# Optimization experiments

Measured on AMD Instinct MI355X. Metric: run time of the kernel, lower is better.

The kernel has to match this reference:

```python
import jax, jax.numpy as jnp
import numpy as np

NJ, NS = 30000, 12000            # num job / skill nodes
E_JS, E_SJ, E_SS = 300000, 300000, 150000
SBERT, HID, OUT = 384, 128, 128
H = 2                             # GAT heads (concat=True)
NEG_SLOPE = 0.2


def setup_inputs() -> dict:
    key = jax.random.key(0)
    ks = iter(jax.random.split(key, 64))
    nrm = lambda shape, s=1.0: jax.random.normal(next(ks), shape, jnp.float32) * s
    ridx = lambda n, hi: jax.random.randint(next(ks), (n,), 0, hi, jnp.int32)
    W = 0.05  # weight scale to keep activations sane across layers
    return dict(
        x_job=nrm((NJ, SBERT)), x_skill=nrm((NS, SBERT)),
        ei_js_src=ridx(E_JS, NJ), ei_js_dst=ridx(E_JS, NS),
        ei_sj_src=ridx(E_SJ, NS), ei_sj_dst=ridx(E_SJ, NJ),
        ei_ss_src=ridx(E_SS, NS), ei_ss_dst=ridx(E_SS, NS),
        query=nrm((SBERT,)),
        W0_job=nrm((SBERT, HID), W), b0_job=jnp.zeros((HID,), jnp.float32),
        g0_job=jnp.ones((HID,), jnp.float32), be0_job=jnp.zeros((HID,), jnp.float32),
        W0_skill=nrm((SBERT, HID), W), b0_skill=jnp.zeros((HID,), jnp.float32),
        g0_skill=jnp.ones((HID,), jnp.float32), be0_skill=jnp.zeros((HID,), jnp.float32),
        gat_Ws=nrm((2, 3, HID, H * HID), W), gat_Wd=nrm((2, 3, HID, H * HID), W),
        gat_as=nrm((2, 3, H, HID), W), gat_ad=nrm((2, 3, H, HID), W),
        gat_b=jnp.zeros((2, 3, H * HID), jnp.float32),
        inter_W=nrm((2, 2, H * HID, HID), W), inter_b=jnp.zeros((2, 2, HID), jnp.float32),
        Wjf=nrm((HID, OUT), W), bjf=jnp.zeros((OUT,), jnp.float32),
        Wq=nrm((SBERT, OUT), W), bq=jnp.zeros((OUT,), jnp.float32),
    )


def _layer_norm(x, g, b):
    mu = x.mean(-1, keepdims=True)
    var = ((x - mu) ** 2).mean(-1, keepdims=True)
    return (x - mu) * jax.lax.rsqrt(var + 1e-5) * g + b


def _gat(x_src, x_dst, src, dst, Ws, Wd, a_s, a_d, bias, num_dst):
    # PyG GATConv: lin_src/lin_dst (no bias), additive attention, scatter-softmax over dst.
    hs = (x_src @ Ws).reshape(-1, H, HID)            # [Ns,H,C]
    hd = (x_dst @ Wd).reshape(-1, H, HID)            # [Nd,H,C]
    e = jax.nn.leaky_relu((hs * a_s).sum(-1)[src] + (hd * a_d).sum(-1)[dst], NEG_SLOPE)  # [E,H]
    m = jax.ops.segment_max(e, dst, num_segments=num_dst)
    p = jnp.exp(e - m[dst])
    den = jax.ops.segment_sum(p, dst, num_segments=num_dst)
    w = p / (den[dst] + 1e-16)                       # [E,H]
    out = jax.ops.segment_sum(hs[src] * w[:, :, None], dst, num_segments=num_dst)
    return out.reshape(num_dst, H * HID) + bias


def _forward(x_job, x_skill, query,
             W0_job, b0_job, g0_job, be0_job, W0_skill, b0_skill, g0_skill, be0_skill,
             gat_Ws, gat_Wd, gat_as, gat_ad, gat_b, inter_W, inter_b, Wjf, bjf, Wq, bq,
             ei_js_src, ei_js_dst, ei_sj_src, ei_sj_dst, ei_ss_src, ei_ss_dst):
    # initial per-type lin + LN + relu (dropout = identity in eval)
    xj = jax.nn.relu(_layer_norm(x_job @ W0_job + b0_job, g0_job, be0_job))
    xs = jax.nn.relu(_layer_norm(x_skill @ W0_skill + b0_skill, g0_skill, be0_skill))
    # skill->skill relation adds self loops (src == dst node type)
    loops = jnp.arange(NS, dtype=jnp.int32)
    ss_src = jnp.concatenate([ei_ss_src, loops])
    ss_dst = jnp.concatenate([ei_ss_dst, loops])
    for i in range(2):  # num_layers
        o_s = (_gat(xj, xs, ei_js_src, ei_js_dst, gat_Ws[i, 0], gat_Wd[i, 0],
                    gat_as[i, 0], gat_ad[i, 0], gat_b[i, 0], NS)
               + _gat(xs, xs, ss_src, ss_dst, gat_Ws[i, 2], gat_Wd[i, 2],
                      gat_as[i, 2], gat_ad[i, 2], gat_b[i, 2], NS))  # HeteroConv aggr='sum'
        o_j = _gat(xs, xj, ei_sj_src, ei_sj_dst, gat_Ws[i, 1], gat_Wd[i, 1],
                   gat_as[i, 1], gat_ad[i, 1], gat_b[i, 1], NJ)
        xj = jax.nn.relu(o_j @ inter_W[i, 0] + inter_b[i, 0])
        xs = jax.nn.relu(o_s @ inter_W[i, 1] + inter_b[i, 1])
    job_emb = xj @ Wjf + bjf                          # [NJ,OUT]
    q = query @ Wq + bq                               # [OUT]
    scores = job_emb @ q                              # [NJ]
    return scores, job_emb, q


def reference(x_job, x_skill, ei_js_src, ei_js_dst, ei_sj_src, ei_sj_dst,
              ei_ss_src, ei_ss_dst, query,
              W0_job, b0_job, g0_job, be0_job, W0_skill, b0_skill, g0_skill, be0_skill,
              gat_Ws, gat_Wd, gat_as, gat_ad, gat_b, inter_W, inter_b,
              Wjf, bjf, Wq, bq):
    return _forward(x_job, x_skill, query,
                    W0_job, b0_job, g0_job, be0_job, W0_skill, b0_skill, g0_skill, be0_skill,
                    gat_Ws, gat_Wd, gat_as, gat_ad, gat_b, inter_W, inter_b, Wjf, bjf, Wq, bq,
                    ei_js_src, ei_js_dst, ei_sj_src, ei_sj_dst, ei_ss_src, ei_ss_dst)
```

## Files before the change

### kernel.cpp

```cpp
#include <hip/hip_runtime.h>
#include <hip/hip_bf16.h>
#include <math.h>

#define NJ 30000
#define NS 12000
#define E_JS 300000
#define E_SJ 300000
#define E_SS 150000
#define ETOT (E_JS + E_SJ + E_SS + NS)
#define NBINS (NS + NJ + NS)
#define NBUK ((NBINS + 63) / 64)
#define SBERT 384
#define HIST_NB 512
#define SCAT_NB 480
#define CAST_MATS 14
#define CAST_BPM 48
#define PREP_CAST (CAST_MATS * CAST_BPM)
#define PREP_WA   (PREP_CAST + 192)
#define PREP_QV   PREP_WA
#define PREP_GB   (PREP_QV + 1)
#define PREP_HIST (PREP_GB + 1)

static inline int cdiv(int a, int b) { return (a + b - 1) / b; }

typedef __attribute__((ext_vector_type(8))) short bf8_t;
typedef __attribute__((ext_vector_type(4))) float f4_t;
typedef unsigned short u16;

__device__ inline float bf2f(unsigned short u) {
    union { unsigned int i; float f; } z; z.i = ((unsigned int)u) << 16; return z.f;
}
__device__ inline unsigned short f2bf(float f) {
    unsigned int x = __float_as_uint(f);
    unsigned int r = (x + 0x7fffu + ((x >> 16) & 1u)) >> 16;
    return (unsigned short)r;
}

__device__ inline void edge_decode(int e, const int* js_src, const int* js_dst,
                                   const int* sj_src, const int* sj_dst,
                                   const int* ss_src, const int* ss_dst,
                                   int& src, int& bin) {
    if (e < E_JS) { src = js_src[e]; bin = js_dst[e]; }
    else if (e < E_JS + E_SJ) { int i = e - E_JS; src = sj_src[i]; bin = NS + sj_dst[i]; }
    else if (e < E_JS + E_SJ + E_SS) { int i = e - E_JS - E_SJ; src = ss_src[i]; bin = NS + NJ + ss_dst[i]; }
    else { int i = e - E_JS - E_SJ - E_SS; src = i; bin = NS + NJ + i; }
}

struct CastT { const float* src; unsigned short* dst; int K; int N; int srcLd; int dstLd; };
struct PrepArgs {
    CastT m[CAST_MATS];
    const float* Ws; const float* as_; const float* Wd; const float* ad_;
    float* wsa; float* wda; int* bcnt;
    const float* query; const float* Wq; const float* bq; float* qv;
    const float* gat_b; float* gbS;
    const int* js_src; const int* js_dst;
    const int* sj_src; const int* sj_dst;
    const int* ss_src; const int* ss_dst;
};

__global__ __launch_bounds__(256) void k_prep(PrepArgs A) {
    __shared__ float ldt[32][33];
    __shared__ int lh[NBUK];
    int b = blockIdx.x;
    if (b < PREP_CAST) {
        int mi = b / CAST_BPM, bx = b % CAST_BPM;
        CastT cm = A.m[mi];
        int tilesN = cm.N >> 5;
        int total = (cm.K >> 5) * tilesN;
        if (bx >= total) return;
        int tk = bx / tilesN, tn = bx % tilesN;
        int k0 = tk * 32, n0 = tn * 32;
        int col = threadIdx.x & 31;
        int row0 = threadIdx.x >> 5;
#pragma unroll
        for (int r = 0; r < 4; ++r) {
            int kk = row0 + r * 8;
            ldt[kk][col] = cm.src[(size_t)(k0 + kk) * cm.srcLd + n0 + col];
        }
        __syncthreads();
#pragma unroll
        for (int r = 0; r < 4; ++r) {
            int nn = row0 + r * 8;
            cm.dst[(size_t)(n0 + nn) * cm.dstLd + k0 + col] = f2bf(ldt[col][nn]);
        }
    } else if (b < PREP_WA) {
        int qw = ((b - PREP_CAST) * 256 + threadIdx.x) >> 4;
        int cl = threadIdx.x & 15;
        if (qw < 2 * 1536) {
            int which = qw / 1536;
            int r = qw % 1536;
            int lr = r / 256;
            int kh = r % 256;
            int k = kh / 2, h = kh % 2;
            const float* W = which ? A.Wd : A.Ws;
            const float* a = which ? A.ad_ : A.as_;
            const float* wrow = W + ((size_t)(lr * 128 + k)) * 256 + h * 128 + cl * 8;
            const float* arow = a + (size_t)(lr * 2 + h) * 128 + cl * 8;
            float4 w0 = *(const float4*)wrow, w1 = *(const float4*)(wrow + 4);
            float4 a0 = *(const float4*)arow, a1 = *(const float4*)(arow + 4);
            float acc = w0.x * a0.x + w0.y * a0.y + w0.z * a0.z + w0.w * a0.w
                      + w1.x * a1.x + w1.y * a1.y + w1.z * a1.z + w1.w * a1.w;
            acc += __shfl_xor(acc, 1, 64);
            acc += __shfl_xor(acc, 2, 64);
            acc += __shfl_xor(acc, 4, 64);
            acc += __shfl_xor(acc, 8, 64);
            if (cl == 0) (which ? A.wda : A.wsa)[lr * 256 + k * 2 + h] = acc;
        }
    } else if (b == PREP_QV) {
        int c = threadIdx.x;
        if (c < 128) {
            float acc = A.bq[c];
            for (int k = 0; k < SBERT; ++k) acc += A.query[k] * A.Wq[(size_t)k * 128 + c];
            A.qv[c] = acc;
        }
    } else if (b == PREP_GB) {
        int c = threadIdx.x;
        if (c < 256) A.gbS[c] = A.gat_b[c] + A.gat_b[512 + c];
    } else {
        int t = threadIdx.x;
        for (int i = t; i < NBUK; i += 256) lh[i] = 0;
        __syncthreads();
        int hb = b - PREP_HIST;
        for (int e = hb * 256 + t; e < ETOT; e += HIST_NB * 256) {
            int src, bin;
            edge_decode(e, A.js_src, A.js_dst, A.sj_src, A.sj_dst, A.ss_src, A.ss_dst, src, bin);
            atomicAdd(&lh[bin >> 6], 1);
        }
        __syncthreads();
        for (int i = t; i < NBUK; i += 256) {
            int v = lh[i];
            if (v) atomicAdd(&A.bcnt[i], v);
        }
    }
}

struct GJob {
    const void* X; const unsigned short* Wt;
    const float* bias; const float* gamma; const float* beta;
    void* Y; int M; int K; int N; int ldY; int srcf32;
    const float* qv; float* sc;
    int aMode = 0;
    const float* wav0 = nullptr; const float* wav1 = nullptr;
    const float* wav2 = nullptr; const float* wav3 = nullptr;
    float* aOut = nullptr; int aStride = 0;
};
struct GPair { GJob a; GJob b; int blocksA; };

template <int EPI>
__device__ void mgemm_body(const GPair& P, int bx) {
    int mb = bx;
    GJob g = (mb < P.blocksA) ? P.a : P.b;
    if (mb >= P.blocksA) mb -= P.blocksA;
    const int row0 = mb * 64;

    __shared__ __align__(16) float As[2][64][32];
    __shared__ __align__(16) unsigned short Bs[2][128][32];
    const int t = threadIdx.x;
    const int wave = t >> 6, lane = t & 63;
    const int q = lane >> 4, c = lane & 15;
    const int K = g.K;
    const float* Xf = (const float*)g.X;

    f4_t acc[8];
#pragma unroll
    for (int nt = 0; nt < 8; ++nt) acc[nt] = (f4_t){0.f, 0.f, 0.f, 0.f};

    auto STAGE = [&](int cur, int k0) {
#pragma unroll
        for (int i = 0; i < 2; ++i) {
            int bi = i * 256 + t;
            int row = bi >> 3, b = bi & 7;
            int ra = row0 + row; ra = (ra < g.M) ? ra : (g.M - 1);
            const float* gsrc = Xf + (size_t)ra * K + k0 + ((b ^ (row & 7)) << 2);
            __builtin_amdgcn_global_load_lds(
                (__attribute__((address_space(1))) void*)gsrc,
                (__attribute__((address_space(3))) void*)((char*)&As[cur][0][0] + ((i * 4 + wave) << 10)),
                16, 0, 0);
        }
#pragma unroll
        for (int i = 0; i < 2; ++i) {
            int bi = i * 256 + t;
            int row = bi >> 2, b = bi & 3;
            const unsigned short* gsrc = g.Wt + (size_t)row * K + k0 + ((b ^ ((row >> 1) & 3)) << 3);
            __builtin_amdgcn_global_load_lds(
                (__attribute__((address_space(1))) void*)gsrc,
                (__attribute__((address_space(3))) void*)((char*)&Bs[cur][0][0] + ((i * 4 + wave) << 10)),
                16, 0, 0);
        }
    };

    auto MF = [&](int cur) {
        const char* Ab = (const char*)&As[cur][0][0];
        const char* Bb = (const char*)&Bs[cur][0][0];
        int r = wave * 16 + c;
        int sw = r & 7;
        f4_t fa0 = *(const f4_t*)(Ab + r * 128 + (((q * 2) ^ sw) << 4));
        f4_t fa1 = *(const f4_t*)(Ab + r * 128 + (((q * 2 + 1) ^ sw) << 4));
        bf8_t af;
        af[0] = (short)f2bf(fa0[0]); af[1] = (short)f2bf(fa0[1]);
        af[2] = (short)f2bf(fa0[2]); af[3] = (short)f2bf(fa0[3]);
        af[4] = (short)f2bf(fa1[0]); af[5] = (short)f2bf(fa1[1]);
        af[6] = (short)f2bf(fa1[2]); af[7] = (short)f2bf(fa1[3]);
#pragma unroll
        for (int nt = 0; nt < 8; ++nt) {
            int rb = nt * 16 + c;
            bf8_t bfr = *(const bf8_t*)(Bb + rb * 64 + ((q ^ ((rb >> 1) & 3)) << 4));
            acc[nt] = __builtin_amdgcn_mfma_f32_16x16x32_bf16(af, bfr, acc[nt], 0, 0, 0);
        }
    };

    STAGE(0, 0);
    int cur = 0;
    for (int k0 = 0; k0 < K; k0 += 32) {
        asm volatile("s_waitcnt vmcnt(0)" ::: "memory");
        __syncthreads();
        if (k0 + 32 < K) STAGE(cur ^ 1, k0 + 32);
        MF(cur);
        cur ^= 1;
    }

    float bcol[8], gcol[8], becol[8];
#pragma unroll
    for (int nt = 0; nt < 8; ++nt) {
        bcol[nt] = g.bias[nt * 16 + c];
        if constexpr (EPI == 3) {
            gcol[nt] = g.gamma[nt * 16 + c];
            becol[nt] = g.beta[nt * 16 + c];
        }
    }

#pragma unroll
    for (int r = 0; r < 4; ++r) {
        int grow = row0 + wave * 16 + q * 4 + r;
        float v[8];
#pragma unroll
        for (int nt = 0; nt < 8; ++nt) v[nt] = acc[nt][r] + bcol[nt];
        if constexpr (EPI == 3) {
            float s = 0.f, ss = 0.f;
#pragma unroll
            for (int nt = 0; nt < 8; ++nt) { s += v[nt]; ss += v[nt] * v[nt]; }
#pragma unroll
            for (int m = 8; m >= 1; m >>= 1) {
                s += __shfl_xor(s, m, 64);
                ss += __shfl_xor(ss, m, 64);
            }
            float mu = s * (1.f / 128.f);
            float var = ss * (1.f / 128.f) - mu * mu;
            float rs = rsqrtf(var + 1e-5f);
#pragma unroll
            for (int nt = 0; nt < 8; ++nt)
                v[nt] = fmaxf((v[nt] - mu) * rs * gcol[nt] + becol[nt], 0.f);
        }
        if (g.aMode > 0) {
            float pa[8];
#pragma unroll
            for (int i = 0; i < 8; ++i) pa[i] = 0.f;
#pragma unroll
            for (int nt = 0; nt < 8; ++nt) {
                int col = nt * 16 + c;
                float2 w0 = *(const float2*)&g.wav0[col * 2];
                pa[0] += v[nt] * w0.x; pa[1] += v[nt] * w0.y;
                if (g.aMode > 1) {
                    float2 w1 = *(const float2*)&g.wav1[col * 2];
                    pa[2] += v[nt] * w1.x; pa[3] += v[nt] * w1.y;
                }
                if (g.aMode > 2) {
                    float2 w2 = *(const float2*)&g.wav2[col * 2];
                    float2 w3 = *(const float2*)&g.wav3[col * 2];
                    pa[4] += v[nt] * w2.x; pa[5] += v[nt] * w2.y;
                    pa[6] += v[nt] * w3.x; pa[7] += v[nt] * w3.y;
                }
            }
#pragma unroll
            for (int m = 8; m >= 1; m >>= 1) {
                pa[0] += __shfl_xor(pa[0], m, 64); pa[1] += __shfl_xor(pa[1], m, 64);
                pa[2] += __shfl_xor(pa[2], m, 64); pa[3] += __shfl_xor(pa[3], m, 64);
                pa[4] += __shfl_xor(pa[4], m, 64); pa[5] += __shfl_xor(pa[5], m, 64);
                pa[6] += __shfl_xor(pa[6], m, 64); pa[7] += __shfl_xor(pa[7], m, 64);
            }
            if (c == 0 && grow < g.M) {
                float* ao = &g.aOut[(size_t)grow * g.aStride];
                ao[0] = pa[0]; ao[1] = pa[1];
                if (g.aMode > 1) { ao[2] = pa[2]; ao[3] = pa[3]; }
                if (g.aMode > 2) { ao[4] = pa[4]; ao[5] = pa[5]; ao[6] = pa[6]; ao[7] = pa[7]; }
            }
        }
        if (grow < g.M) {
            unsigned short* Y = (unsigned short*)g.Y;
#pragma unroll
            for (int nt = 0; nt < 8; ++nt)
                Y[(size_t)grow * g.ldY + nt * 16 + c] = f2bf(v[nt]);
        }
    }
}

__global__ __launch_bounds__(256) void k_scan(
    const int* __restrict__ bcnt, int* __restrict__ bukoff, int* __restrict__ bukcur) {
    __shared__ int sd[256];
    int t = threadIdx.x;
    int i0 = t * 4;
    int v0 = (i0 < NBUK) ? bcnt[i0] : 0;
    int v1 = (i0 + 1 < NBUK) ? bcnt[i0 + 1] : 0;
    int v2 = (i0 + 2 < NBUK) ? bcnt[i0 + 2] : 0;
    int v3 = (i0 + 3 < NBUK) ? bcnt[i0 + 3] : 0;
    int csum = v0 + v1 + v2 + v3;
    sd[t] = csum;
    __syncthreads();
    for (int off = 1; off < 256; off <<= 1) {
        int tmp = (t >= off) ? sd[t - off] : 0;
        __syncthreads();
        sd[t] += tmp;
        __syncthreads();
    }
    int excl = sd[t] - csum;
    int p0 = excl, p1 = excl + v0, p2 = excl + v0 + v1, p3 = excl + v0 + v1 + v2;
    if (i0 < NBUK) { bukoff[i0] = p0; bukcur[i0] = p0; }
    if (i0 + 1 < NBUK) { bukoff[i0 + 1] = p1; bukcur[i0 + 1] = p1; }
    if (i0 + 2 < NBUK) { bukoff[i0 + 2] = p2; bukcur[i0 + 2] = p2; }
    if (i0 + 3 < NBUK) { bukoff[i0 + 3] = p3; bukcur[i0 + 3] = p3; }
    if (t == 0) bukoff[NBUK] = ETOT;
}

__global__ __launch_bounds__(256) void k_lin0_scat(
    GPair P, int gemmBlocks,
    const int* __restrict__ js_src, const int* __restrict__ js_dst,
    const int* __restrict__ sj_src, const int* __restrict__ sj_dst,
    const int* __restrict__ ss_src, const int* __restrict__ ss_dst,
    int* __restrict__ bukcur, uint2* __restrict__ pairs) {
    if (blockIdx.x < (unsigned)gemmBlocks) {
        mgemm_body<3>(P, blockIdx.x);
        return;
    }
    __shared__ int lh[NBUK];
    __shared__ int lbase[NBUK];
    int t = threadIdx.x;
    int sb = blockIdx.x - gemmBlocks;
    const int CH = (ETOT + SCAT_NB - 1) / SCAT_NB;
    const int beg = sb * CH;
    const int endi = (beg + CH < ETOT) ? beg + CH : ETOT;
    if (beg >= ETOT) return;
    for (int i = t; i < NBUK; i += 256) lh[i] = 0;
    __syncthreads();
    for (int e = beg + t; e < endi; e += 256) {
        int src, bin;
        edge_decode(e, js_src, js_dst, sj_src, sj_dst, ss_src, ss_dst, src, bin);
        atomicAdd(&lh[bin >> 6], 1);
    }
    __syncthreads();
    for (int i = t; i < NBUK; i += 256) {
        int v = lh[i];
        lbase[i] = v ? atomicAdd(&bukcur[i], v) : 0;
    }
    __syncthreads();
    for (int i = t; i < NBUK; i += 256) lh[i] = 0;
    __syncthreads();
    for (int e = beg + t; e < endi; e += 256) {
        int src, bin;
        edge_decode(e, js_src, js_dst, sj_src, sj_dst, ss_src, ss_dst, src, bin);
        int bu = bin >> 6;
        int pos = lbase[bu] + atomicAdd(&lh[bu], 1);
        pairs[pos] = make_uint2((unsigned)src, (unsigned)bin);
    }
}

__global__ __launch_bounds__(256) void k_finalize(
    const uint2* __restrict__ pairs, const int* __restrict__ bukoff,
    int* __restrict__ offs, int* __restrict__ esrc) {
    int b = blockIdx.x, t = threadIdx.x;
    int base = bukoff[b], endi = bukoff[b + 1];
    __shared__ int cnt[64], excl[64], curs[64];
    if (t < 64) cnt[t] = 0;
    __syncthreads();
    for (int i = base + t; i < endi; i += 256)
        atomicAdd(&cnt[pairs[i].y & 63], 1);
    __syncthreads();
    if (t < 64) {
        int v = cnt[t];
        int inc = v;
#pragma unroll
        for (int off = 1; off < 64; off <<= 1) {
            int tmp = __shfl_up(inc, off, 64);
            if (t >= off) inc += tmp;
        }
        excl[t] = inc - v;
        curs[t] = inc - v;
    }
    __syncthreads();
    for (int i = base + t; i < endi; i += 256) {
        uint2 p = pairs[i];
        int lb = p.y & 63;
        int pos = atomicAdd(&curs[lb], 1);
        esrc[base + pos] = (int)p.x;
    }
    if (t < 64) {
        int bin = b * 64 + t;
        if (bin < NBINS) offs[bin] = base + excl[t];
    }
    if (b == 0 && t == 0) offs[NBINS] = ETOT;
}

__device__ inline void fm8(float p0, float p1, uint4 u, float a0[8], float a1[8]) {
    float x0 = __uint_as_float(u.x << 16);
    float x1 = __uint_as_float(u.x & 0xffff0000u);
    float x2 = __uint_as_float(u.y << 16);
    float x3 = __uint_as_float(u.y & 0xffff0000u);
    float x4 = __uint_as_float(u.z << 16);
    float x5 = __uint_as_float(u.z & 0xffff0000u);
    float x6 = __uint_as_float(u.w << 16);
    float x7 = __uint_as_float(u.w & 0xffff0000u);
    a0[0] += p0 * x0; a0[1] += p0 * x1; a0[2] += p0 * x2; a0[3] += p0 * x3;
    a0[4] += p0 * x4; a0[5] += p0 * x5; a0[6] += p0 * x6; a0[7] += p0 * x7;
    a1[0] += p1 * x0; a1[1] += p1 * x1; a1[2] += p1 * x2; a1[3] += p1 * x3;
    a1[4] += p1 * x4; a1[5] += p1 * x5; a1[6] += p1 * x6; a1[7] += p1 * x7;
}

__device__ inline void rel_run(
    const int* __restrict__ esrc, int beg, int end,
    const float* __restrict__ aSrc, int aShift, int aOff, float adx, float ady,
    const unsigned short* __restrict__ rows, int colOff, int g,
    float a0[8], float a1[8], float& den0, float& den1) {
    int j = beg;
    for (; j + 8 <= end; j += 8) {
        int s0 = esrc[j + g];
        int s1 = esrc[j + 4 + g];
        uint4 u0 = *(const uint4*)&rows[(unsigned)s0 * 128 + colOff];
        uint4 u1 = *(const uint4*)&rows[(unsigned)s1 * 128 + colOff];
        float2 f0 = *(const float2*)&aSrc[((unsigned)s0 << aShift) + aOff];
        float2 f1 = *(const float2*)&aSrc[((unsigned)s1 << aShift) + aOff];
        float e00 = f0.x + adx; e00 = e00 > 0.f ? e00 : 0.2f * e00;
        float e01 = f0.y + ady; e01 = e01 > 0.f ? e01 : 0.2f * e01;
        float e10 = f1.x + adx; e10 = e10 > 0.f ? e10 : 0.2f * e10;
        float e11 = f1.y + ady; e11 = e11 > 0.f ? e11 : 0.2f * e11;
        float p00 = __expf(e00), p01 = __expf(e01);
        float p10 = __expf(e10), p11 = __expf(e11);
        fm8(p00, p01, u0, a0, a1);
        fm8(p10, p11, u1, a0, a1);
        den0 += p00 + p10; den1 += p01 + p11;
    }
    for (; j < end; j += 4) {
        int e = j + g;
        bool ok = e < end;
        int s = esrc[ok ? e : j];
        uint4 u = *(const uint4*)&rows[(unsigned)s * 128 + colOff];
        float2 f = *(const float2*)&aSrc[((unsigned)s << aShift) + aOff];
        float e0 = f.x + adx; e0 = e0 > 0.f ? e0 : 0.2f * e0;
        float e1 = f.y + ady; e1 = e1 > 0.f ? e1 : 0.2f * e1;
        float p0 = ok ? __expf(e0) : 0.f;
        float p1 = ok ? __expf(e1) : 0.f;
        fm8(p0, p1, u, a0, a1);
        den0 += p0; den1 += p1;
    }
}

__device__ inline void store8(unsigned short* dst, const float v[8]) {
    uint4 o;
    o.x = (unsigned)f2bf(v[0]) | ((unsigned)f2bf(v[1]) << 16);
    o.y = (unsigned)f2bf(v[2]) | ((unsigned)f2bf(v[3]) << 16);
    o.z = (unsigned)f2bf(v[4]) | ((unsigned)f2bf(v[5]) << 16);
    o.w = (unsigned)f2bf(v[6]) | ((unsigned)f2bf(v[7]) << 16);
    *(uint4*)dst = o;
}

__device__ inline void finish_store(float a0[8], float a1[8], float den0, float den1,
                                    int lane, unsigned short* base) {
    float d0 = den0; d0 += __shfl_xor(d0, 16, 64); d0 += __shfl_xor(d0, 32, 64);
    float d1 = den1; d1 += __shfl_xor(d1, 16, 64); d1 += __shfl_xor(d1, 32, 64);
    float s0 = 1.f / (d0 + 1e-16f), s1 = 1.f / (d1 + 1e-16f);
    float o0[8], o1[8];
#pragma unroll
    for (int i = 0; i < 8; ++i) {
        float t0 = a0[i]; t0 += __shfl_xor(t0, 16, 64); t0 += __shfl_xor(t0, 32, 64);
        float t1 = a1[i]; t1 += __shfl_xor(t1, 16, 64); t1 += __shfl_xor(t1, 32, 64);
        o0[i] = t0 * s0; o1[i] = t1 * s1;
    }
    if ((lane >> 4) == 0) {
        store8(base, o0);
        store8(base + 128, o1);
    }
}

__global__ __launch_bounds__(256) void k_gather_all(
    const int* __restrict__ offs, const int* __restrict__ esrc,
    const float* __restrict__ aJ, const float* __restrict__ aS,
    const unsigned short* __restrict__ rowsJ,
    const unsigned short* __restrict__ rowsS,
    unsigned short* __restrict__ aggS,
    unsigned short* __restrict__ aggJ,
    int jobOnly) {
    int wave = threadIdx.x >> 6, lane = threadIdx.x & 63;
    int idx = blockIdx.x * 4 + wave;
    int g = lane >> 4, cl = lane & 15;
    int colOff = cl * 8;

    float a0[8], a1[8], den0, den1;

    if (jobOnly) {
        if (idx >= NJ) return;
        int d = idx;
#pragma unroll
        for (int i = 0; i < 8; ++i) { a0[i] = 0.f; a1[i] = 0.f; }
        den0 = den1 = 0.f;
        int bb = NS + d;
        float2 ad = *(const float2*)&aJ[(unsigned)d * 4 + 2];
        rel_run(esrc, offs[bb], offs[bb + 1], aS, 3, 4, ad.x, ad.y, rowsS, colOff, g, a0, a1, den0, den1);
        finish_store(a0, a1, den0, den1, lane, &aggJ[(size_t)d * 256 + colOff]);
        return;
    }
    if (idx < NS) {
        int d = idx;
#pragma unroll
        for (int i = 0; i < 8; ++i) { a0[i] = 0.f; a1[i] = 0.f; }
        den0 = den1 = 0.f;
        float2 adA = *(const float2*)&aS[(unsigned)d * 8 + 2];
        rel_run(esrc, offs[d], offs[d + 1], aJ, 2, 0, adA.x, adA.y, rowsJ, colOff, g, a0, a1, den0, den1);
        finish_store(a0, a1, den0, den1, lane, &aggS[(size_t)d * 512 + colOff]);
#pragma unroll
        for (int i = 0; i < 8; ++i) { a0[i] = 0.f; a1[i] = 0.f; }
        den0 = den1 = 0.f;
        int bb = NS + NJ + d;
        float2 adB = *(const float2*)&aS[(unsigned)d * 8 + 6];
        rel_run(esrc, offs[bb], offs[bb + 1], aS, 3, 0, adB.x, adB.y, rowsS, colOff, g, a0, a1, den0, den1);
        finish_store(a0, a1, den0, den1, lane, &aggS[(size_t)d * 512 + 256 + colOff]);
    } else if (idx < NS + NJ) {
        int d = idx - NS;
#pragma unroll
        for (int i = 0; i < 8; ++i) { a0[i] = 0.f; a1[i] = 0.f; }
        den0 = den1 = 0.f;
        int bb = NS + d;
        float2 ad = *(const float2*)&aJ[(unsigned)d * 4 + 2];
        rel_run(esrc, offs[bb], offs[bb + 1], aS, 3, 4, ad.x, ad.y, rowsS, colOff, g, a0, a1, den0, den1);
        finish_store(a0, a1, den0, den1, lane, &aggJ[(size_t)d * 256 + colOff]);
    }
}

struct FJob {
    const unsigned short* X; int K1; int M;
    const unsigned short* Wt1; const float* bias1;
    const unsigned short* Wt2; const float* bias2;
    const float* wa; float* aOut; int aStride;
    unsigned short* Y2;
};
struct FPair { FJob a; FJob b; int blocksA; };

__global__ __launch_bounds__(256) void k_fused2(FPair P) {
    int mb = blockIdx.x;
    FJob g = (mb < P.blocksA) ? P.a : P.b;
    if (mb >= P.blocksA) mb -= P.blocksA;
    const int row0 = mb * 64;
    const int K1 = g.K1;

    __shared__ __align__(16) unsigned short Al[64][40];
    __shared__ __align__(16) unsigned short Bl[256][40];
    __shared__ __align__(16) unsigned short Y1l[4][64][40];
    const int t = threadIdx.x;
    const int wave = t >> 6, lane = t & 63;
    const int q = lane >> 4, c = lane & 15;

    f4_t acc0[8], acc1[8], acc2[8];
#pragma unroll
    for (int nt = 0; nt < 8; ++nt) {
        acc0[nt] = (f4_t){0.f, 0.f, 0.f, 0.f};
        acc1[nt] = (f4_t){0.f, 0.f, 0.f, 0.f};
        acc2[nt] = (f4_t){0.f, 0.f, 0.f, 0.f};
    }

    for (int k0 = 0; k0 < K1; k0 += 32) {
#pragma unroll
        for (int it = 0; it < 5; ++it) {
            int idx = t + it * 256;
            int r = idx >> 2, cc = (idx & 3) * 8;
            if (r < 64) {
                int gr = row0 + r;
                uint4 va = (gr < g.M) ? *(const uint4*)&g.X[(size_t)gr * K1 + k0 + cc]
                                      : make_uint4(0u, 0u, 0u, 0u);
                *(uint4*)&Al[r][cc] = va;
            } else {
                int br = r - 64;
                *(uint4*)&Bl[br][cc] = *(const uint4*)&g.Wt1[(size_t)br * K1 + k0 + cc];
            }
        }
        __syncthreads();
        bf8_t af = *(const bf8_t*)&Al[wave * 16 + c][q * 8];
#pragma unroll
        for (int nt = 0; nt < 8; ++nt) {
            bf8_t b0 = *(const bf8_t*)&Bl[nt * 16 + c][q * 8];
            acc0[nt] = __builtin_amdgcn_mfma_f32_16x16x32_bf16(af, b0, acc0[nt], 0, 0, 0);
            bf8_t b1 = *(const bf8_t*)&Bl[128 + nt * 16 + c][q * 8];
            acc1[nt] = __builtin_amdgcn_mfma_f32_16x16x32_bf16(af, b1, acc1[nt], 0, 0, 0);
        }
        __syncthreads();
    }

#pragma unroll
    for (int np = 0; np < 2; ++np) {
        float bcol[8];
#pragma unroll
        for (int nt = 0; nt < 8; ++nt) bcol[nt] = g.bias1[np * 128 + nt * 16 + c];
#pragma unroll
        for (int r = 0; r < 4; ++r) {
            int row = wave * 16 + q * 4 + r;
#pragma unroll
            for (int nt = 0; nt < 8; ++nt) {
                float vv = (np ? acc1[nt][r] : acc0[nt][r]) + bcol[nt];
                Y1l[nt >> 1][row][(nt & 1) * 16 + c] = f2bf(vv);
            }
        }
        __syncthreads();
        for (int k0 = 0; k0 < 128; k0 += 32) {
#pragma unroll
            for (int it = 0; it < 2; ++it) {
                int idx = t + it * 256;
                int br = idx >> 2, cc = (idx & 3) * 8;
                *(uint4*)&Bl[br][cc] = *(const uint4*)&g.Wt2[(size_t)br * 256 + np * 128 + k0 + cc];
            }
            __syncthreads();
            bf8_t af = *(const bf8_t*)&Y1l[k0 >> 5][wave * 16 + c][q * 8];
#pragma unroll
            for (int nt = 0; nt < 8; ++nt) {
                bf8_t bfr = *(const bf8_t*)&Bl[nt * 16 + c][q * 8];
                acc2[nt] = __builtin_amdgcn_mfma_f32_16x16x32_bf16(af, bfr, acc2[nt], 0, 0, 0);
            }
            __syncthreads();
        }
    }

    float b2[8];
#pragma unroll
    for (int nt = 0; nt < 8; ++nt) b2[nt] = g.bias2[nt * 16 + c];
#pragma unroll
    for (int r = 0; r < 4; ++r) {
        int grow = row0 + wave * 16 + q * 4 + r;
        float v[8];
#pragma unroll
        for (int nt = 0; nt < 8; ++nt) v[nt] = fmaxf(acc2[nt][r] + b2[nt], 0.f);
        if (g.wa) {
            float pa0 = 0.f, pa1 = 0.f;
#pragma unroll
            for (int nt = 0; nt < 8; ++nt) {
                float2 w0 = *(const float2*)&g.wa[(nt * 16 + c) * 2];
                pa0 += v[nt] * w0.x; pa1 += v[nt] * w0.y;
            }
#pragma unroll
            for (int m = 8; m >= 1; m >>= 1) {
                pa0 += __shfl_xor(pa0, m, 64);
                pa1 += __shfl_xor(pa1, m, 64);
            }
            if (c == 0 && grow < g.M) {
                g.aOut[(size_t)grow * g.aStride + 0] = pa0;
                g.aOut[(size_t)grow * g.aStride + 1] = pa1;
            }
        }
        if (g.Y2 && grow < g.M) {
#pragma unroll
            for (int nt = 0; nt < 8; ++nt)
                g.Y2[(size_t)grow * 128 + nt * 16 + c] = f2bf(v[nt]);
        }
    }
}

struct F3 {
    const unsigned short* X; int M;
    const unsigned short* Wt1; const float* bias1;
    const unsigned short* Wt2; const float* bias2;
    const unsigned short* Wt3; const float* bias3;
    const float* qv; float* sc; float* Y;
};

__global__ __launch_bounds__(256) void k_fused3(F3 g) {
    int mb = blockIdx.x;
    const int row0 = mb * 64;
    __shared__ __align__(16) unsigned short Al[64][40];
    __shared__ __align__(16) unsigned short Bl[256][40];
    __shared__ __align__(16) unsigned short Yl[4][64][40];
    const int t = threadIdx.x;
    const int wave = t >> 6, lane = t & 63;
    const int q = lane >> 4, c = lane & 15;

    f4_t acc0[8], acc1[8], acc2[8];
#pragma unroll
    for (int nt = 0; nt < 8; ++nt) {
        acc0[nt] = (f4_t){0.f, 0.f, 0.f, 0.f};
        acc1[nt] = (f4_t){0.f, 0.f, 0.f, 0.f};
        acc2[nt] = (f4_t){0.f, 0.f, 0.f, 0.f};
    }

    for (int k0 = 0; k0 < 256; k0 += 32) {
#pragma unroll
        for (int it = 0; it < 5; ++it) {
            int idx = t + it * 256;
            int r = idx >> 2, cc = (idx & 3) * 8;
            if (r < 64) {
                int gr = row0 + r;
                uint4 va = (gr < g.M) ? *(const uint4*)&g.X[(size_t)gr * 256 + k0 + cc]
                                      : make_uint4(0u, 0u, 0u, 0u);
                *(uint4*)&Al[r][cc] = va;
            } else {
                int br = r - 64;
                *(uint4*)&Bl[br][cc] = *(const uint4*)&g.Wt1[(size_t)br * 256 + k0 + cc];
            }
        }
        __syncthreads();
        bf8_t af = *(const bf8_t*)&Al[wave * 16 + c][q * 8];
#pragma unroll
        for (int nt = 0; nt < 8; ++nt) {
            bf8_t b0 = *(const bf8_t*)&Bl[nt * 16 + c][q * 8];
            acc0[nt] = __builtin_amdgcn_mfma_f32_16x16x32_bf16(af, b0, acc0[nt], 0, 0, 0);
            bf8_t b1 = *(const bf8_t*)&Bl[128 + nt * 16 + c][q * 8];
            acc1[nt] = __builtin_amdgcn_mfma_f32_16x16x32_bf16(af, b1, acc1[nt], 0, 0, 0);
        }
        __syncthreads();
    }

#pragma unroll
    for (int np = 0; np < 2; ++np) {
        float bcol[8];
#pragma unroll
        for (int nt = 0; nt < 8; ++nt) bcol[nt] = g.bias1[np * 128 + nt * 16 + c];
#pragma unroll
        for (int r = 0; r < 4; ++r) {
            int row = wave * 16 + q * 4 + r;
#pragma unroll
            for (int nt = 0; nt < 8; ++nt) {
                float vv = (np ? acc1[nt][r] : acc0[nt][r]) + bcol[nt];
                Yl[nt >> 1][row][(nt & 1) * 16 + c] = f2bf(vv);
            }
        }
        __syncthreads();
        for (int k0 = 0; k0 < 128; k0 += 32) {
#pragma unroll
            for (int it = 0; it < 2; ++it) {
                int idx = t + it * 256;
                int br = idx >> 2, cc = (idx & 3) * 8;
                *(uint4*)&Bl[br][cc] = *(const uint4*)&g.Wt2[(size_t)br * 256 + np * 128 + k0 + cc];
            }
            __syncthreads();
            bf8_t af = *(const bf8_t*)&Yl[k0 >> 5][wave * 16 + c][q * 8];
#pragma unroll
            for (int nt = 0; nt < 8; ++nt) {
                bf8_t bfr = *(const bf8_t*)&Bl[nt * 16 + c][q * 8];
                acc2[nt] = __builtin_amdgcn_mfma_f32_16x16x32_bf16(af, bfr, acc2[nt], 0, 0, 0);
            }
            __syncthreads();
        }
    }

    {
        float b2[8];
#pragma unroll
        for (int nt = 0; nt < 8; ++nt) b2[nt] = g.bias2[nt * 16 + c];
#pragma unroll
        for (int r = 0; r < 4; ++r) {
            int row = wave * 16 + q * 4 + r;
#pragma unroll
            for (int nt = 0; nt < 8; ++nt)
                Yl[nt >> 1][row][(nt & 1) * 16 + c] = f2bf(fmaxf(acc2[nt][r] + b2[nt], 0.f));
        }
        __syncthreads();
    }

    f4_t acc3[8];
#pragma unroll
    for (int nt = 0; nt < 8; ++nt) acc3[nt] = (f4_t){0.f, 0.f, 0.f, 0.f};
    for (int k0 = 0; k0 < 128; k0 += 32) {
#pragma unroll
        for (int it = 0; it < 2; ++it) {
            int idx = t + it * 256;
            int br = idx >> 2, cc = (idx & 3) * 8;
            *(uint4*)&Bl[br][cc] = *(const uint4*)&g.Wt3[(size_t)br * 128 + k0 + cc];
        }
        __syncthreads();
        bf8_t af = *(const bf8_t*)&Yl[k0 >> 5][wave * 16 + c][q * 8];
#pragma unroll
        for (int nt = 0; nt < 8; ++nt) {
            bf8_t bfr = *(const bf8_t*)&Bl[nt * 16 + c][q * 8];
            acc3[nt] = __builtin_amdgcn_mfma_f32_16x16x32_bf16(af, bfr, acc3[nt], 0, 0, 0);
        }
        __syncthreads();
    }
    float b3[8], qcol[8];
#pragma unroll
    for (int nt = 0; nt < 8; ++nt) {
        b3[nt] = g.bias3[nt * 16 + c];
        qcol[nt] = g.qv[nt * 16 + c];
    }
#pragma unroll
    for (int r = 0; r < 4; ++r) {
        int grow = row0 + wave * 16 + q * 4 + r;
        float v[8];
#pragma unroll
        for (int nt = 0; nt < 8; ++nt) v[nt] = acc3[nt][r] + b3[nt];
        float part = 0.f;
#pragma unroll
        for (int nt = 0; nt < 8; ++nt) part += v[nt] * qcol[nt];
#pragma unroll
        for (int m = 8; m >= 1; m >>= 1) part += __shfl_xor(part, m, 64);
        if (grow < g.M) {
            if (c == 0) g.sc[grow] = part;
#pragma unroll
            for (int nt = 0; nt < 8; ++nt)
                g.Y[(size_t)grow * 128 + nt * 16 + c] = v[nt];
        }
    }
}

extern "C" void kernel_launch(void* const* d_in, const int* in_sizes, int n_in,
                              void* d_out, int out_size, void* d_ws, size_t ws_size,
                              hipStream_t stream) {
    const float* x_job   = (const float*)d_in[0];
    const float* x_skill = (const float*)d_in[1];
    const int* js_src = (const int*)d_in[2];
    const int* js_dst = (const int*)d_in[3];
    const int* sj_src = (const int*)d_in[4];
    const int* sj_dst = (const int*)d_in[5];
    const int* ss_src = (const int*)d_in[6];
    const int* ss_dst = (const int*)d_in[7];
    const float* query    = (const float*)d_in[8];
    const float* W0_job   = (const float*)d_in[9];
    const float* b0_job   = (const float*)d_in[10];
    const float* g0_job   = (const float*)d_in[11];
    const float* be0_job  = (const float*)d_in[12];
    const float* W0_skill = (const float*)d_in[13];
    const float* b0_skill = (const float*)d_in[14];
    const float* g0_skill = (const float*)d_in[15];
    const float* be0_skill= (const float*)d_in[16];
    const float* gat_Ws = (const float*)d_in[17];
    const float* gat_Wd = (const float*)d_in[18];
    const float* gat_as = (const float*)d_in[19];
    const float* gat_ad = (const float*)d_in[20];
    const float* gat_b  = (const float*)d_in[21];
    const float* inter_W = (const float*)d_in[22];
    const float* inter_b = (const float*)d_in[23];
    const float* Wjf = (const float*)d_in[24];
    const float* bjf = (const float*)d_in[25];
    const float* Wq  = (const float*)d_in[26];
    const float* bq  = (const float*)d_in[27];

    char* w = (char*)d_ws;
    auto alloc = [&](size_t bytes) -> void* {
        void* p = (void*)w;
        w += (bytes + 255) & ~(size_t)255;
        return p;
    };
    u16* xj   = (u16*)alloc((size_t)NJ * 128 * 2);
    u16* xs   = (u16*)alloc((size_t)NS * 128 * 2);
    u16* xs1  = (u16*)alloc((size_t)NS * 128 * 2);
    u16* aggJ  = (u16*)alloc((size_t)NJ * 256 * 2);
    u16* aggJ1 = (u16*)alloc((size_t)NJ * 256 * 2);
    u16* aggS  = (u16*)alloc((size_t)NS * 512 * 2);
    u16* WtW0j = (u16*)alloc((size_t)SBERT * 128 * 2);
    u16* WtW0s = (u16*)alloc((size_t)SBERT * 128 * 2);
    u16* WsS1  = (u16*)alloc((size_t)256 * 512 * 2);
    u16* WsJ0  = (u16*)alloc((size_t)256 * 256 * 2);
    u16* WsJ1  = (u16*)alloc((size_t)256 * 256 * 2);
    u16* WtI00 = (u16*)alloc((size_t)128 * 256 * 2);
    u16* WtI01 = (u16*)alloc((size_t)128 * 256 * 2);
    u16* WtI10 = (u16*)alloc((size_t)128 * 256 * 2);
    u16* WtJf  = (u16*)alloc((size_t)128 * 128 * 2);
    float* gbS = (float*)alloc(256 * 4);
    float* aJ = (float*)alloc((size_t)NJ * 4 * 4);
    float* aS = (float*)alloc((size_t)NS * 8 * 4);
    float* wsa = (float*)alloc(6 * 256 * 4);
    float* wda = (float*)alloc(6 * 256 * 4);
    int* bcnt   = (int*)alloc((size_t)NBUK * 4);
    int* bukoff = (int*)alloc((size_t)(NBUK + 1) * 4);
    int* bukcur = (int*)alloc((size_t)NBUK * 4);
    uint2* pairs = (uint2*)alloc((size_t)ETOT * 8);
    int* offs = (int*)alloc((size_t)(NBINS + 1) * 4);
    int* esrc = (int*)alloc((size_t)ETOT * 4);

    float* out = (float*)d_out;
    float* scores  = out;
    float* job_emb = out + NJ;
    float* qv      = out + NJ + (size_t)NJ * 128;

    const int mbJ = cdiv(NJ, 64);
    const int mbS = cdiv(NS, 64);
    const int gemmB = mbJ + mbS;

    hipMemsetAsync(bcnt, 0, (size_t)NBUK * 4, stream);
    hipMemsetAsync(WsS1, 0, (size_t)256 * 512 * 2, stream);
    hipMemsetAsync(WsJ0, 0, (size_t)256 * 256 * 2, stream);
    hipMemsetAsync(WsJ1, 0, (size_t)256 * 256 * 2, stream);

    {
        const size_t WS = (size_t)128 * 256;
        const size_t IW = (size_t)256 * 128;
        PrepArgs A;
        A.m[0]  = {W0_job,   WtW0j, SBERT, 128, 128, SBERT};
        A.m[1]  = {W0_skill, WtW0s, SBERT, 128, 128, SBERT};
        A.m[2]  = {gat_Ws + 0 * WS,       WsS1,                       128, 128, 256, 512};
        A.m[3]  = {gat_Ws + 0 * WS + 128, WsS1 + 128 * 512 + 128,     128, 128, 256, 512};
        A.m[4]  = {gat_Ws + 2 * WS,       WsS1 + 256,                 128, 128, 256, 512};
        A.m[5]  = {gat_Ws + 2 * WS + 128, WsS1 + 128 * 512 + 384,     128, 128, 256, 512};
        A.m[6]  = {gat_Ws + 1 * WS,       WsJ0,                       128, 128, 256, 256};
        A.m[7]  = {gat_Ws + 1 * WS + 128, WsJ0 + 128 * 256 + 128,     128, 128, 256, 256};
        A.m[8]  = {gat_Ws + 4 * WS,       WsJ1,                       128, 128, 256, 256};
        A.m[9]  = {gat_Ws + 4 * WS + 128, WsJ1 + 128 * 256 + 128,     128, 128, 256, 256};
        A.m[10] = {inter_W + 0 * IW, WtI00, 256, 128, 128, 256};
        A.m[11] = {inter_W + 1 * IW, WtI01, 256, 128, 128, 256};
        A.m[12] = {inter_W + 2 * IW, WtI10, 256, 128, 128, 256};
        A.m[13] = {Wjf, WtJf, 128, 128, 128, 128};
        A.Ws = gat_Ws; A.as_ = gat_as; A.Wd = gat_Wd; A.ad_ = gat_ad;
        A.wsa = wsa; A.wda = wda; A.bcnt = bcnt;
        A.query = query; A.Wq = Wq; A.bq = bq; A.qv = qv;
        A.gat_b = gat_b; A.gbS = gbS;
        A.js_src = js_src; A.js_dst = js_dst;
        A.sj_src = sj_src; A.sj_dst = sj_dst;
        A.ss_src = ss_src; A.ss_dst = ss_dst;
        k_prep<<<PREP_HIST + HIST_NB, 256, 0, stream>>>(A);
    }

    k_scan<<<1, 256, 0, stream>>>(bcnt, bukoff, bukcur);

    {
        GPair P;
        P.a = {x_job, WtW0j, b0_job, g0_job, be0_job, xj, NJ, SBERT, 128, 128, 1,
               nullptr, nullptr, 2, wsa + 0, wda + 256, nullptr, nullptr, aJ, 4};
        P.b = {x_skill, WtW0s, b0_skill, g0_skill, be0_skill, xs, NS, SBERT, 128, 128, 1,
               nullptr, nullptr, 4, wsa + 2 * 256, wda + 0, wsa + 1 * 256, wda + 2 * 256, aS, 8};
        P.blocksA = mbJ;
        k_lin0_scat<<<gemmB + SCAT_NB, 256, 0, stream>>>(
            P, gemmB, js_src, js_dst, sj_src, sj_dst, ss_src, ss_dst, bukcur, pairs);
    }

    k_finalize<<<NBUK, 256, 0, stream>>>(pairs, bukoff, offs, esrc);

    k_gather_all<<<cdiv(NS + NJ, 4), 256, 0, stream>>>(
        offs, esrc, aJ, aS, xj, xs, aggS, aggJ, 0);

    {
        FPair P;
        P.a = {aggJ, 256, NJ, WsJ0, gat_b + 256, WtI00, inter_b + 0,
               wda + 4 * 256, aJ + 2, 4, nullptr};
        P.b = {aggS, 512, NS, WsS1, gbS, WtI01, inter_b + 128,
               wsa + 4 * 256, aS + 4, 8, xs1};
        P.blocksA = mbJ;
        k_fused2<<<gemmB, 256, 0, stream>>>(P);
    }

    k_gather_all<<<cdiv(NJ, 4), 256, 0, stream>>>(
        offs, esrc, aJ, aS, nullptr, xs1, nullptr, aggJ1, 1);

    {
        F3 g3;
        g3.X = aggJ1; g3.M = NJ;
        g3.Wt1 = WsJ1; g3.bias1 = gat_b + 4 * 256;
        g3.Wt2 = WtI10; g3.bias2 = inter_b + 2 * 128;
        g3.Wt3 = WtJf; g3.bias3 = bjf;
        g3.qv = qv; g3.sc = scores; g3.Y = job_emb;
        k_fused3<<<mbJ, 256, 0, stream>>>(g3);
    }
}
```

Before: 332.1 us.

## Replace two-level bucketed CSR build with direct per-bin counting sort

The CSR construction used to run a 64-bin bucket histogram, bucket scatter of (src,bin) pairs, and a finalize kernel that sorted within buckets. It is replaced by a per-bin global atomic histogram, a single-block scan over all 54k bins, and a direct atomic scatter of source ids into esrc. This removes one kernel launch and the intermediate pairs buffer. In exchange it relies on heavy global atomics, and the single-block scan now loops serially over about 211 bins per thread.

```diff
diff --git a/kernel.cpp b/kernel.cpp
--- a/kernel.cpp
+++ b/kernel.cpp
@@ -9,7 +9,6 @@
 #define E_SS 150000
 #define ETOT (E_JS + E_SJ + E_SS + NS)
 #define NBINS (NS + NJ + NS)
-#define NBUK ((NBINS + 63) / 64)
 #define SBERT 384
 #define HIST_NB 512
 #define SCAT_NB 480
@@ -60,7 +59,6 @@
 
 __global__ __launch_bounds__(256) void k_prep(PrepArgs A) {
     __shared__ float ldt[32][33];
-    __shared__ int lh[NBUK];
     int b = blockIdx.x;
     if (b < PREP_CAST) {
         int mi = b / CAST_BPM, bx = b % CAST_BPM;
@@ -117,19 +115,11 @@
         int c = threadIdx.x;
         if (c < 256) A.gbS[c] = A.gat_b[c] + A.gat_b[512 + c];
     } else {
-        int t = threadIdx.x;
-        for (int i = t; i < NBUK; i += 256) lh[i] = 0;
-        __syncthreads();
         int hb = b - PREP_HIST;
-        for (int e = hb * 256 + t; e < ETOT; e += HIST_NB * 256) {
+        for (int e = hb * 256 + threadIdx.x; e < ETOT; e += HIST_NB * 256) {
             int src, bin;
             edge_decode(e, A.js_src, A.js_dst, A.sj_src, A.sj_dst, A.ss_src, A.ss_dst, src, bin);
-            atomicAdd(&lh[bin >> 6], 1);
-        }
-        __syncthreads();
-        for (int i = t; i < NBUK; i += 256) {
-            int v = lh[i];
-            if (v) atomicAdd(&A.bcnt[i], v);
+            atomicAdd(&A.bcnt[bin], 1);
         }
     }
 }
@@ -295,30 +285,30 @@
 }
 
 __global__ __launch_bounds__(256) void k_scan(
-    const int* __restrict__ bcnt, int* __restrict__ bukoff, int* __restrict__ bukcur) {
-    __shared__ int sd[256];
+    const int* __restrict__ bcnt, int* __restrict__ offs, int* __restrict__ cur) {
+    __shared__ int sums[256];
     int t = threadIdx.x;
-    int i0 = t * 4;
-    int v0 = (i0 < NBUK) ? bcnt[i0] : 0;
-    int v1 = (i0 + 1 < NBUK) ? bcnt[i0 + 1] : 0;
-    int v2 = (i0 + 2 < NBUK) ? bcnt[i0 + 2] : 0;
-    int v3 = (i0 + 3 < NBUK) ? bcnt[i0 + 3] : 0;
-    int csum = v0 + v1 + v2 + v3;
-    sd[t] = csum;
+    const int CH = (NBINS + 255) / 256;
+    int b0 = t * CH;
+    int e0 = b0 + CH; if (e0 > NBINS) e0 = NBINS;
+    int s = 0;
+    for (int i = b0; i < e0; ++i) s += bcnt[i];
+    sums[t] = s;
     __syncthreads();
     for (int off = 1; off < 256; off <<= 1) {
-        int tmp = (t >= off) ? sd[t - off] : 0;
-        __syncthreads();
-        sd[t] += tmp;
-        __syncthreads();
-    }
-    int excl = sd[t] - csum;
-    int p0 = excl, p1 = excl + v0, p2 = excl + v0 + v1, p3 = excl + v0 + v1 + v2;
-    if (i0 < NBUK) { bukoff[i0] = p0; bukcur[i0] = p0; }
-    if (i0 + 1 < NBUK) { bukoff[i0 + 1] = p1; bukcur[i0 + 1] = p1; }
-    if (i0 + 2 < NBUK) { bukoff[i0 + 2] = p2; bukcur[i0 + 2] = p2; }
-    if (i0 + 3 < NBUK) { bukoff[i0 + 3] = p3; bukcur[i0 + 3] = p3; }
-    if (t == 0) bukoff[NBUK] = ETOT;
+        int tmp = (t >= off) ? sums[t - off] : 0;
+        __syncthreads();
+        sums[t] += tmp;
+        __syncthreads();
+    }
+    int run = sums[t] - s;
+    for (int i = b0; i < e0; ++i) {
+        int v = bcnt[i];
+        offs[i] = run;
+        cur[i] = run;
+        run += v;
+    }
+    if (t == 255) offs[NBINS] = ETOT;
 }
 
 __global__ __launch_bounds__(256) void k_lin0_scat(
@@ -326,77 +316,23 @@
     const int* __restrict__ js_src, const int* __restrict__ js_dst,
     const int* __restrict__ sj_src, const int* __restrict__ sj_dst,
     const int* __restrict__ ss_src, const int* __restrict__ ss_dst,
-    int* __restrict__ bukcur, uint2* __restrict__ pairs) {
+    int* __restrict__ cur, int* __restrict__ esrc) {
     if (blockIdx.x < (unsigned)gemmBlocks) {
         mgemm_body<3>(P, blockIdx.x);
         return;
     }
-    __shared__ int lh[NBUK];
-    __shared__ int lbase[NBUK];
     int t = threadIdx.x;
     int sb = blockIdx.x - gemmBlocks;
     const int CH = (ETOT + SCAT_NB - 1) / SCAT_NB;
     const int beg = sb * CH;
     const int endi = (beg + CH < ETOT) ? beg + CH : ETOT;
     if (beg >= ETOT) return;
-    for (int i = t; i < NBUK; i += 256) lh[i] = 0;
-    __syncthreads();
     for (int e = beg + t; e < endi; e += 256) {
         int src, bin;
         edge_decode(e, js_src, js_dst, sj_src, sj_dst, ss_src, ss_dst, src, bin);
-        atomicAdd(&lh[bin >> 6], 1);
-    }
-    __syncthreads();
-    for (int i = t; i < NBUK; i += 256) {
-        int v = lh[i];
-        lbase[i] = v ? atomicAdd(&bukcur[i], v) : 0;
-    }
-    __syncthreads();
-    for (int i = t; i < NBUK; i += 256) lh[i] = 0;
-    __syncthreads();
-    for (int e = beg + t; e < endi; e += 256) {
-        int src, bin;
-        edge_decode(e, js_src, js_dst, sj_src, sj_dst, ss_src, ss_dst, src, bin);
-        int bu = bin >> 6;
-        int pos = lbase[bu] + atomicAdd(&lh[bu], 1);
-        pairs[pos] = make_uint2((unsigned)src, (unsigned)bin);
-    }
-}
-
-__global__ __launch_bounds__(256) void k_finalize(
-    const uint2* __restrict__ pairs, const int* __restrict__ bukoff,
-    int* __restrict__ offs, int* __restrict__ esrc) {
-    int b = blockIdx.x, t = threadIdx.x;
-    int base = bukoff[b], endi = bukoff[b + 1];
-    __shared__ int cnt[64], excl[64], curs[64];
-    if (t < 64) cnt[t] = 0;
-    __syncthreads();
-    for (int i = base + t; i < endi; i += 256)
-        atomicAdd(&cnt[pairs[i].y & 63], 1);
-    __syncthreads();
-    if (t < 64) {
-        int v = cnt[t];
-        int inc = v;
-#pragma unroll
-        for (int off = 1; off < 64; off <<= 1) {
-            int tmp = __shfl_up(inc, off, 64);
-            if (t >= off) inc += tmp;
-        }
-        excl[t] = inc - v;
-        curs[t] = inc - v;
-    }
-    __syncthreads();
-    for (int i = base + t; i < endi; i += 256) {
-        uint2 p = pairs[i];
-        int lb = p.y & 63;
-        int pos = atomicAdd(&curs[lb], 1);
-        esrc[base + pos] = (int)p.x;
-    }
-    if (t < 64) {
-        int bin = b * 64 + t;
-        if (bin < NBINS) offs[bin] = base + excl[t];
-    }
-    if (b == 0 && t == 0) offs[NBINS] = ETOT;
+        int pos = atomicAdd(&cur[bin], 1);
+        esrc[pos] = src;
+    }
 }
 
 __device__ inline void fm8(float p0, float p1, uint4 u, float a0[8], float a1[8]) {
@@ -861,11 +797,9 @@
     float* aS = (float*)alloc((size_t)NS * 8 * 4);
     float* wsa = (float*)alloc(6 * 256 * 4);
     float* wda = (float*)alloc(6 * 256 * 4);
-    int* bcnt   = (int*)alloc((size_t)NBUK * 4);
-    int* bukoff = (int*)alloc((size_t)(NBUK + 1) * 4);
-    int* bukcur = (int*)alloc((size_t)NBUK * 4);
-    uint2* pairs = (uint2*)alloc((size_t)ETOT * 8);
+    int* bcnt = (int*)alloc((size_t)NBINS * 4);
     int* offs = (int*)alloc((size_t)(NBINS + 1) * 4);
+    int* curb = (int*)alloc((size_t)NBINS * 4);
     int* esrc = (int*)alloc((size_t)ETOT * 4);
 
     float* out = (float*)d_out;
@@ -877,7 +811,7 @@
     const int mbS = cdiv(NS, 64);
     const int gemmB = mbJ + mbS;
 
-    hipMemsetAsync(bcnt, 0, (size_t)NBUK * 4, stream);
+    hipMemsetAsync(bcnt, 0, (size_t)NBINS * 4, stream);
     hipMemsetAsync(WsS1, 0, (size_t)256 * 512 * 2, stream);
     hipMemsetAsync(WsJ0, 0, (size_t)256 * 256 * 2, stream);
     hipMemsetAsync(WsJ1, 0, (size_t)256 * 256 * 2, stream);
@@ -910,7 +844,7 @@
         k_prep<<<PREP_HIST + HIST_NB, 256, 0, stream>>>(A);
     }
 
-    k_scan<<<1, 256, 0, stream>>>(bcnt, bukoff, bukcur);
+    k_scan<<<1, 256, 0, stream>>>(bcnt, offs, curb);
 
     {
         GPair P;
@@ -920,10 +854,8 @@
                nullptr, nullptr, 4, wsa + 2 * 256, wda + 0, wsa + 1 * 256, wda + 2 * 256, aS, 8};
         P.blocksA = mbJ;
         k_lin0_scat<<<gemmB + SCAT_NB, 256, 0, stream>>>(
-            P, gemmB, js_src, js_dst, sj_src, sj_dst, ss_src, ss_dst, bukcur, pairs);
-    }
-
-    k_finalize<<<NBUK, 256, 0, stream>>>(pairs, bukoff, offs, esrc);
+            P, gemmB, js_src, js_dst, sj_src, sj_dst, ss_src, ss_dst, curb, esrc);
+    }
 
     k_gather_all<<<cdiv(NS + NJ, 4), 256, 0, stream>>>(
         offs, esrc, aJ, aS, xj, xs, aggS, aggJ, 0);
```

After: 489.6 us. 1.47x slower.
